# Kernel tuning notes

Hardware: AMD Instinct MI355X
Metric: run time of the kernel (lower is better)

Reference implementation:

```python
import jax, jax.numpy as jnp
import numpy as np
import math

B, N, D, H = 4, 2048, 1024, 16
HD = D // H  # head dim = 64


def setup_inputs() -> dict:
    key = jax.random.key(0)
    ks = jax.random.split(key, 5)
    x = jax.random.normal(ks[0], (B, N, D), dtype=jnp.float32)
    # per-head kqv Linear: weight (3*HD, D), bias (3*HD), stacked over heads
    Wkqv = jax.random.normal(ks[1], (H, 3 * HD, D), dtype=jnp.float32) / math.sqrt(D)
    bkqv = jax.random.normal(ks[2], (H, 3 * HD), dtype=jnp.float32) * 0.02
    # output projection Linear(D, D)
    Wproj = jax.random.normal(ks[3], (D, D), dtype=jnp.float32) / math.sqrt(D)
    bproj = jax.random.normal(ks[4], (D,), dtype=jnp.float32) * 0.02
    return {"x": x, "Wkqv": Wkqv, "bkqv": bkqv, "Wproj": Wproj, "bproj": bproj}


def reference(x, Wkqv, bkqv, Wproj, bproj):
    # per-head linear: y = x @ W.T + b  -> [B, H, N, 3*HD]
    kqv = jnp.einsum('bnd,hed->bhne', x, Wkqv) + bkqv[None, :, None, :]
    k, q, v = jnp.split(kqv, 3, axis=-1)  # each [B, H, N, HD]
    # scores = q @ k^T / sqrt(HD)   (attention_scores(k, q) -> q @ k.T)
    scores = jnp.einsum('bhqd,bhkd->bhqk', q, k) / math.sqrt(HD)
    causal = jnp.tril(jnp.ones((N, N), dtype=bool))
    scores = jnp.where(causal[None, None], scores, -jnp.inf)
    att = jax.nn.softmax(scores, axis=-1)
    out = jnp.einsum('bhqk,bhkd->bhqd', att, v)  # [B, H, N, HD]
    # concat heads: [B, N, H*HD]
    sa = out.transpose(0, 2, 1, 3).reshape(B, N, D)
    # dropout is identity in eval mode; final projection
    return sa @ Wproj.T + bproj
```

## Files before the change

kernel.cpp:

```cpp
#include <hip/hip_runtime.h>
#include <hip/hip_bf16.h>


#define NSEQ 2048
#define NHEAD 16
#define DMODEL 1024
#define SCALE2 0.18033688011112042f

typedef __attribute__((ext_vector_type(8))) short v8s;
typedef __attribute__((ext_vector_type(4))) float v4f;

__device__ __forceinline__ float bf2f(unsigned short u) {
    union { unsigned int i; float f; } v;
    v.i = ((unsigned int)u) << 16;
    return v.f;
}
__device__ __forceinline__ unsigned short f2bf(float f) {
    unsigned int x = __float_as_uint(f);
    return (unsigned short)((x + 0x7fffu + ((x >> 16) & 1u)) >> 16);
}
__device__ __forceinline__ unsigned short f2bf_rh(float f) {
    return (unsigned short)((__float_as_uint(f) + 0x8000u) >> 16);
}
__device__ __forceinline__ float fast_exp2(float x) {
#if __has_builtin(__builtin_amdgcn_exp2f)
    return __builtin_amdgcn_exp2f(x);
#else
    return __expf(x * 0.69314718056f);
#endif
}
__device__ __forceinline__ void gld_lds16(const unsigned short* g, unsigned short* l) {
    __builtin_amdgcn_global_load_lds(
        (const __attribute__((address_space(1))) void*)g,
        (__attribute__((address_space(3))) void*)l, 16, 0, 0);
}

__global__ __launch_bounds__(256) void cvt_bf16(
    const float* __restrict__ x, const float* __restrict__ wk, const float* __restrict__ wp,
    unsigned short* __restrict__ xb, unsigned short* __restrict__ wkb,
    unsigned short* __restrict__ wpb)
{
    const int i = blockIdx.x * 256 + threadIdx.x;
    const float* s; unsigned short* d; int o;
    if (i < 2097152)      { s = x;  d = xb;  o = i; }
    else if (i < 2883584) {
        s = wk; d = wkb;
        const int oi  = i - 2097152;
        const int row = oi >> 8, cq = oi & 255;
        const int h   = row / 192;
        const int rem = row - h * 192;
        const int cls = rem >> 6, e = rem & 63;
        float4 f = ((const float4*)s)[oi];
        ushort4 u;
        u.x = f2bf(f.x); u.y = f2bf(f.y); u.z = f2bf(f.z); u.w = f2bf(f.w);
        ((ushort4*)d)[(((cls << 10) + (h << 6) + e) << 8) + cq] = u;
        return;
    }
    else                  { s = wp; d = wpb; o = i - 2883584; }
    float4 f = ((const float4*)s)[o];
    ushort4 u;
    u.x = f2bf(f.x); u.y = f2bf(f.y); u.z = f2bf(f.z); u.w = f2bf(f.w);
    ((ushort4*)d)[o] = u;
}

template <int EPI>
__global__ __launch_bounds__(512, 2) void gemm_lds(
    const unsigned short* __restrict__ A, const unsigned short* __restrict__ B,
    const float* __restrict__ bias,
    float* __restrict__ Cf,
    unsigned short* __restrict__ Kb, unsigned short* __restrict__ Qb,
    unsigned short* __restrict__ VTb,
    int M, int Nc, int K)
{
    __shared__ __align__(16) unsigned short Al[4][8192];
    __shared__ __align__(16) unsigned short Bl[4][8192];

    const int t = threadIdx.x, wave = t >> 6, lane = t & 63;
    const int wm = wave >> 2, wn = wave & 3;

    const int lin = blockIdx.y * gridDim.x + blockIdx.x;
    const int xcd = lin & 7, pos = lin >> 3;
    const int by  = (xcd << 2) + (pos & 3);
    const int bx  = pos >> 2;
    const int m0 = by * 256, n0 = bx * 256;
    const int quad = lane >> 4, c = lane & 15;

    const int g0 = wave * 2, g1 = wave * 2 + 1;
    const int r15 = lane & 15, kg = (lane >> 4) & 3;
    const unsigned short* sA0 = A + (size_t)(m0 + g0 * 16 + r15) * K + kg * 8;
    const unsigned short* sA1 = A + (size_t)(m0 + g1 * 16 + r15) * K + kg * 8;
    const unsigned short* sB0 = B + (size_t)(n0 + g0 * 16 + r15) * K + kg * 8;
    const unsigned short* sB1 = B + (size_t)(n0 + g1 * 16 + r15) * K + kg * 8;

    v4f acc[8][4];
#pragma unroll
    for (int i = 0; i < 8; ++i)
#pragma unroll
        for (int j = 0; j < 4; ++j) acc[i][j] = (v4f){0.f, 0.f, 0.f, 0.f};

    const int fbase = (quad * 16 + c) * 8;
    const int nt = K >> 5;

    auto stageA = [&](int sl, int tt) {
        const int o = tt << 5;
        unsigned short* la = &Al[sl][0];
        gld_lds16(sA0 + o, la + g0 * 512);
        gld_lds16(sA1 + o, la + g1 * 512);
    };
    auto stageB = [&](int sl, int tt) {
        const int o = tt << 5;
        unsigned short* lb = &Bl[sl][0];
        gld_lds16(sB0 + o, lb + g0 * 512);
        gld_lds16(sB1 + o, lb + g1 * 512);
    };

    stageA(0, 0); stageB(0, 0);
    stageA(1, 1); stageB(1, 1);
    stageA(2, 2); stageB(2, 2);
    asm volatile("s_waitcnt vmcnt(8)" ::: "memory");
    __builtin_amdgcn_s_barrier();

    for (int tt = 0; tt < nt; ++tt) {
        const int sl  = tt & 3;
        const int sl3 = (tt + 3) & 3;
        const bool pf = (tt + 3 < nt);

        v8s bfr[4], af[4];
#pragma unroll
        for (int ns = 0; ns < 4; ++ns)
            bfr[ns] = *(const v8s*)&Bl[sl][(wn * 4 + ns) * 512 + fbase];
#pragma unroll
        for (int ms = 0; ms < 4; ++ms)
            af[ms] = *(const v8s*)&Al[sl][(wm * 8 + ms) * 512 + fbase];
        if (pf) stageA(sl3, tt + 3);
        __builtin_amdgcn_s_barrier();
        asm volatile("s_waitcnt lgkmcnt(0)" ::: "memory");
        __builtin_amdgcn_s_setprio(1);
#pragma unroll
        for (int ms = 0; ms < 4; ++ms)
#pragma unroll
            for (int ns = 0; ns < 4; ++ns)
                acc[ms][ns] = __builtin_amdgcn_mfma_f32_16x16x32_bf16(
                    af[ms], bfr[ns], acc[ms][ns], 0, 0, 0);
        __builtin_amdgcn_s_setprio(0);
        __builtin_amdgcn_s_barrier();

        v8s af2[4];
#pragma unroll
        for (int ms = 0; ms < 4; ++ms)
            af2[ms] = *(const v8s*)&Al[sl][(wm * 8 + 4 + ms) * 512 + fbase];
        if (pf) stageB(sl3, tt + 3);
        __builtin_amdgcn_s_barrier();
        asm volatile("s_waitcnt lgkmcnt(0)" ::: "memory");
        __builtin_amdgcn_s_setprio(1);
#pragma unroll
        for (int ms = 0; ms < 4; ++ms)
#pragma unroll
            for (int ns = 0; ns < 4; ++ns)
                acc[4 + ms][ns] = __builtin_amdgcn_mfma_f32_16x16x32_bf16(
                    af2[ms], bfr[ns], acc[4 + ms][ns], 0, 0, 0);
        __builtin_amdgcn_s_setprio(0);
        if (pf)                   { asm volatile("s_waitcnt vmcnt(8)" ::: "memory"); }
        else if (tt + 2 < nt)     { asm volatile("s_waitcnt vmcnt(4)" ::: "memory"); }
        else                      { asm volatile("s_waitcnt vmcnt(0)" ::: "memory"); }
        __builtin_amdgcn_s_barrier();
    }

#pragma unroll
    for (int ms = 0; ms < 8; ++ms) {
        const int row0 = m0 + wm * 128 + ms * 16 + quad * 4;
#pragma unroll
        for (int ns = 0; ns < 4; ++ns) {
            const int colbase = n0 + wn * 64 + ns * 16;
            float bn, scl = 1.f;
            if (EPI == 2) {
                bn = bias[colbase + c];
            } else {
                const int cls = colbase >> 10;
                const int wi  = colbase & 1023;
                const int h   = wi >> 6, e0 = wi & 63;
                bn = bias[h * 192 + cls * 64 + e0 + c];
                if (cls == 1) scl = SCALE2;
            }
            float v0 = (acc[ms][ns][0] + bn) * scl;
            float v1 = (acc[ms][ns][1] + bn) * scl;
            float v2 = (acc[ms][ns][2] + bn) * scl;
            float v3 = (acc[ms][ns][3] + bn) * scl;
            if (EPI == 2) {
                float* pc = Cf + (size_t)row0 * Nc + colbase + c;
                pc[0] = v0; pc[(size_t)Nc] = v1;
                pc[(size_t)2 * Nc] = v2; pc[(size_t)3 * Nc] = v3;
            } else {
                const int cls = colbase >> 10;
                const int wi  = colbase & 1023;
                const int h   = wi >> 6, e = (wi & 63) + c;
                const int bb  = row0 >> 11, tok0 = row0 & 2047;
                const int bhh = bb * 16 + h;
                if (cls == 2) {
                    ushort4 pk;
                    pk.x = f2bf(v0); pk.y = f2bf(v1); pk.z = f2bf(v2); pk.w = f2bf(v3);
                    *(ushort4*)(VTb + ((size_t)bhh * 64 + e) * 2048 + tok0) = pk;
                } else {
                    unsigned short* dst = (cls == 0) ? Kb : Qb;
                    const size_t base = ((size_t)bhh * 2048 + tok0) * 64 + e;
                    dst[base]       = f2bf(v0);
                    dst[base + 64]  = f2bf(v1);
                    dst[base + 128] = f2bf(v2);
                    dst[base + 192] = f2bf(v3);
                }
            }
        }
    }
}

template <bool A_BF16, int EPI>
__global__ __launch_bounds__(256) void gemm_mfma(
    const void* __restrict__ Av, const float* __restrict__ B,
    const float* __restrict__ bias,
    float* __restrict__ Cf,
    unsigned short* __restrict__ Kb, unsigned short* __restrict__ Qb,
    unsigned short* __restrict__ VTb,
    int M, int Nc, int K)
{
    __shared__ __align__(16) unsigned short Al[512 * 8];
    __shared__ __align__(16) unsigned short Bl[512 * 8];

    const int t = threadIdx.x;
    const int wave = t >> 6, lane = t & 63;
    const int wm = wave >> 1, wn = wave & 1;
    const int m0 = blockIdx.y * 128, n0 = blockIdx.x * 128;
    const int quad = lane >> 4, c = lane & 15;

    const int srow = t >> 1, skh = t & 1;
    const int sslot = (srow >> 4) * 64 + (skh * 2) * 16 + (srow & 15);

    v4f acc[4][4];
#pragma unroll
    for (int i = 0; i < 4; ++i)
#pragma unroll
        for (int j = 0; j < 4; ++j) acc[i][j] = (v4f){0.f, 0.f, 0.f, 0.f};

    const unsigned short* pa_u = (const unsigned short*)Av + (size_t)(m0 + srow) * K + skh * 16;
    const float*          pa_f = (const float*)Av          + (size_t)(m0 + srow) * K + skh * 16;
    const float*          pb   = B                          + (size_t)(n0 + srow) * K + skh * 16;

    const int fbase = (quad * 16 + c) * 8;

    for (int k0 = 0; k0 < K; k0 += 32) {
        unsigned short a16[16], b16[16];
        if (A_BF16) {
            uint4 r0 = *(const uint4*)(pa_u + k0);
            uint4 r1 = *(const uint4*)(pa_u + k0 + 8);
            *(uint4*)&a16[0] = r0; *(uint4*)&a16[8] = r1;
        } else {
            float4 f0 = *(const float4*)(pa_f + k0);
            float4 f1 = *(const float4*)(pa_f + k0 + 4);
            float4 f2 = *(const float4*)(pa_f + k0 + 8);
            float4 f3 = *(const float4*)(pa_f + k0 + 12);
            a16[0] = f2bf_rh(f0.x); a16[1] = f2bf_rh(f0.y); a16[2] = f2bf_rh(f0.z); a16[3] = f2bf_rh(f0.w);
            a16[4] = f2bf_rh(f1.x); a16[5] = f2bf_rh(f1.y); a16[6] = f2bf_rh(f1.z); a16[7] = f2bf_rh(f1.w);
            a16[8] = f2bf_rh(f2.x); a16[9] = f2bf_rh(f2.y); a16[10] = f2bf_rh(f2.z); a16[11] = f2bf_rh(f2.w);
            a16[12] = f2bf_rh(f3.x); a16[13] = f2bf_rh(f3.y); a16[14] = f2bf_rh(f3.z); a16[15] = f2bf_rh(f3.w);
        }
        {
            float4 g0 = *(const float4*)(pb + k0);
            float4 g1 = *(const float4*)(pb + k0 + 4);
            float4 g2 = *(const float4*)(pb + k0 + 8);
            float4 g3 = *(const float4*)(pb + k0 + 12);
            b16[0] = f2bf_rh(g0.x); b16[1] = f2bf_rh(g0.y); b16[2] = f2bf_rh(g0.z); b16[3] = f2bf_rh(g0.w);
            b16[4] = f2bf_rh(g1.x); b16[5] = f2bf_rh(g1.y); b16[6] = f2bf_rh(g1.z); b16[7] = f2bf_rh(g1.w);
            b16[8] = f2bf_rh(g2.x); b16[9] = f2bf_rh(g2.y); b16[10] = f2bf_rh(g2.z); b16[11] = f2bf_rh(g2.w);
            b16[12] = f2bf_rh(g3.x); b16[13] = f2bf_rh(g3.y); b16[14] = f2bf_rh(g3.z); b16[15] = f2bf_rh(g3.w);
        }
        __syncthreads();
        *(uint4*)&Al[sslot * 8]        = *(uint4*)&a16[0];
        *(uint4*)&Al[(sslot + 16) * 8] = *(uint4*)&a16[8];
        *(uint4*)&Bl[sslot * 8]        = *(uint4*)&b16[0];
        *(uint4*)&Bl[(sslot + 16) * 8] = *(uint4*)&b16[8];
        __syncthreads();

        v8s af[4], bf[4];
#pragma unroll
        for (int ms = 0; ms < 4; ++ms)
            af[ms] = *(const v8s*)&Al[(wm * 4 + ms) * 512 + fbase];
#pragma unroll
        for (int ns = 0; ns < 4; ++ns)
            bf[ns] = *(const v8s*)&Bl[(wn * 4 + ns) * 512 + fbase];
#pragma unroll
        for (int ms = 0; ms < 4; ++ms)
#pragma unroll
            for (int ns = 0; ns < 4; ++ns)
                acc[ms][ns] = __builtin_amdgcn_mfma_f32_16x16x32_bf16(
                    af[ms], bf[ns], acc[ms][ns], 0, 0, 0);
    }

#pragma unroll
    for (int ms = 0; ms < 4; ++ms) {
        const int row0 = m0 + wm * 64 + ms * 16 + quad * 4;
#pragma unroll
        for (int ns = 0; ns < 4; ++ns) {
            const int colbase = n0 + wn * 64 + ns * 16;
            float bn = (EPI == 2) ? bias[colbase + c] : bias[colbase + c];
            float v0 = acc[ms][ns][0] + bn;
            float v1 = acc[ms][ns][1] + bn;
            float v2 = acc[ms][ns][2] + bn;
            float v3 = acc[ms][ns][3] + bn;
            if (EPI == 2) {
                float* pc = Cf + (size_t)row0 * Nc + colbase + c;
                pc[0] = v0; pc[(size_t)Nc] = v1;
                pc[(size_t)2 * Nc] = v2; pc[(size_t)3 * Nc] = v3;
            } else {
                const int hh = colbase / 192;
                const int eb = colbase - hh * 192;
                const int bb = row0 >> 11, tok0 = row0 & 2047;
                const int bhh = bb * 16 + hh;
                if (eb >= 128) {
                    ushort4 pk;
                    pk.x = f2bf(v0); pk.y = f2bf(v1); pk.z = f2bf(v2); pk.w = f2bf(v3);
                    *(ushort4*)(VTb + ((size_t)bhh * 64 + (eb - 128) + c) * 2048 + tok0) = pk;
                } else {
                    const bool isq = (eb >= 64);
                    const float s = isq ? SCALE2 : 1.f;
                    unsigned short* dst = isq ? Qb : Kb;
                    const int e = (isq ? eb - 64 : eb) + c;
                    const size_t base = ((size_t)bhh * 2048 + tok0) * 64 + e;
                    dst[base]       = f2bf(v0 * s);
                    dst[base + 64]  = f2bf(v1 * s);
                    dst[base + 128] = f2bf(v2 * s);
                    dst[base + 192] = f2bf(v3 * s);
                }
            }
        }
    }
}

#define ATTS 72

__global__ __launch_bounds__(256, 2) void attn_mfma(
    const unsigned short* __restrict__ Kbuf,
    const unsigned short* __restrict__ Qbuf,
    const unsigned short* __restrict__ VT,
    unsigned short* __restrict__ sa)
{
    __shared__ __align__(16) unsigned short Ps[4][2][64 * ATTS];

    const int t = threadIdx.x, w = t >> 6, lane = t & 63;
    const int quad = lane >> 4, c = lane & 15;
    const int bh = blockIdx.x & 63, bq = blockIdx.x >> 6;
    const int b = bh >> 4, hh = bh & 15;
    const int qt = (w == 0) ? bq : (w == 1) ? (15 - bq) : (w == 2) ? (16 + bq) : (31 - bq);
    const int qw = qt * 64;
    const size_t gbase = (size_t)bh * (2048 * 64);

    const int rs  = c & 3;
    const int rc0 = (quad ^ rs) * 8, rc1 = 32 + rc0;
    unsigned short* PsW0 = &Ps[w][0][0];
    unsigned short* PsW1 = &Ps[w][1][0];

    v8s qf[4][2];
#pragma unroll
    for (int qs = 0; qs < 4; ++qs) {
        const unsigned short* qp = Qbuf + gbase + (size_t)(qw + qs * 16 + c) * 64 + quad * 8;
        qf[qs][0] = *(const v8s*)qp;
        qf[qs][1] = *(const v8s*)(qp + 32);
    }
    v4f oacc[4][4], lacc[4];
#pragma unroll
    for (int qs = 0; qs < 4; ++qs) {
        lacc[qs] = (v4f){0.f, 0.f, 0.f, 0.f};
#pragma unroll
        for (int dn = 0; dn < 4; ++dn) oacc[qs][dn] = (v4f){0.f, 0.f, 0.f, 0.f};
    }
    const short oneb = (short)0x3F80;
    const v8s ones = {oneb, oneb, oneb, oneb, oneb, oneb, oneb, oneb};

    const int nkt = qt + 1;
    for (int kt = 0; kt < nkt; ++kt) {
        const int kbase = kt * 64;
        const bool diag = (kt == nkt - 1);
        unsigned short* PsW = (kt & 1) ? PsW1 : PsW0;

        v8s vf[4][2];
#pragma unroll
        for (int dn = 0; dn < 4; ++dn) {
            const unsigned short* vp =
                VT + gbase + (size_t)(dn * 16 + c) * 2048 + kbase + quad * 8;
            vf[dn][0] = *(const v8s*)vp;
            vf[dn][1] = *(const v8s*)(vp + 32);
        }

#pragma unroll
        for (int kn = 0; kn < 4; ++kn) {
            const unsigned short* kp =
                Kbuf + gbase + (size_t)(kbase + kn * 16 + c) * 64 + quad * 8;
            v8s kf0 = *(const v8s*)kp;
            v8s kf1 = *(const v8s*)(kp + 32);
#pragma unroll
            for (int qs = 0; qs < 4; ++qs) {
                v4f s = (v4f){0.f, 0.f, 0.f, 0.f};
                s = __builtin_amdgcn_mfma_f32_16x16x32_bf16(qf[qs][0], kf0, s, 0, 0, 0);
                s = __builtin_amdgcn_mfma_f32_16x16x32_bf16(qf[qs][1], kf1, s, 0, 0, 0);
                if (diag) {
#pragma unroll
                    for (int r = 0; r < 4; ++r)
                        if (kn * 16 + c > qs * 16 + quad * 4 + r) s[r] = -1e30f;
                }
#pragma unroll
                for (int r = 0; r < 4; ++r) {
                    const float p = fast_exp2(s[r]);
                    PsW[(qs * 16 + quad * 4 + r) * ATTS +
                        (((2 * kn + (c >> 3)) ^ r) * 8) + (c & 7)] = f2bf_rh(p);
                }
            }
        }
        v8s pa[4][2];
#pragma unroll
        for (int qs = 0; qs < 4; ++qs) {
            pa[qs][0] = *(const v8s*)&PsW[(qs * 16 + c) * ATTS + rc0];
            pa[qs][1] = *(const v8s*)&PsW[(qs * 16 + c) * ATTS + rc1];
        }
#pragma unroll
        for (int dn = 0; dn < 4; ++dn) {
#pragma unroll
            for (int qs = 0; qs < 4; ++qs) {
                oacc[qs][dn] = __builtin_amdgcn_mfma_f32_16x16x32_bf16(pa[qs][0], vf[dn][0], oacc[qs][dn], 0, 0, 0);
                oacc[qs][dn] = __builtin_amdgcn_mfma_f32_16x16x32_bf16(pa[qs][1], vf[dn][1], oacc[qs][dn], 0, 0, 0);
            }
        }
#pragma unroll
        for (int qs = 0; qs < 4; ++qs) {
            lacc[qs] = __builtin_amdgcn_mfma_f32_16x16x32_bf16(pa[qs][0], ones, lacc[qs], 0, 0, 0);
            lacc[qs] = __builtin_amdgcn_mfma_f32_16x16x32_bf16(pa[qs][1], ones, lacc[qs], 0, 0, 0);
        }
    }

#pragma unroll
    for (int qs = 0; qs < 4; ++qs) {
        float inv[4];
#pragma unroll
        for (int r = 0; r < 4; ++r) inv[r] = 1.f / lacc[qs][r];
        const size_t obase =
            ((size_t)(b * 2048 + qw + qs * 16 + quad * 4)) * DMODEL + hh * 64;
#pragma unroll
        for (int dn = 0; dn < 4; ++dn)
#pragma unroll
            for (int r = 0; r < 4; ++r)
                sa[obase + (size_t)r * DMODEL + dn * 16 + c] = f2bf(oacc[qs][dn][r] * inv[r]);
    }
}

extern "C" void kernel_launch(void* const* d_in, const int* in_sizes, int n_in,
                              void* d_out, int out_size, void* d_ws, size_t ws_size,
                              hipStream_t stream) {
    const float* x     = (const float*)d_in[0];
    const float* Wkqv  = (const float*)d_in[1];
    const float* bkqv  = (const float*)d_in[2];
    const float* Wproj = (const float*)d_in[3];
    const float* bproj = (const float*)d_in[4];
    float* out = (float*)d_out;

    unsigned short* Kb = (unsigned short*)d_ws;
    unsigned short* Qb = Kb + (size_t)8388608;
    unsigned short* VT = Qb + (size_t)8388608;
    unsigned short* sa = VT + (size_t)8388608;

    const bool fast = ws_size >= 75497472ull;
    if (fast) {
        unsigned short* xb  = sa;
        unsigned short* wkb = (unsigned short*)d_ws + (size_t)33554432;
        unsigned short* wpb = wkb + (size_t)3145728;
        cvt_bf16<<<12288, 256, 0, stream>>>(x, Wkqv, Wproj, xb, wkb, wpb);
        gemm_lds<1><<<dim3(12, 32), 512, 0, stream>>>(
            xb, wkb, bkqv, nullptr, Kb, Qb, VT, 8192, 3072, 1024);
        attn_mfma<<<512, 256, 0, stream>>>(Kb, Qb, VT, sa);
        gemm_lds<2><<<dim3(4, 32), 512, 0, stream>>>(
            sa, wpb, bproj, out, nullptr, nullptr, nullptr, 8192, 1024, 1024);
    } else {
        gemm_mfma<false, 1><<<dim3(24, 64), 256, 0, stream>>>(
            x, Wkqv, bkqv, nullptr, Kb, Qb, VT, 8192, 3072, 1024);
        attn_mfma<<<512, 256, 0, stream>>>(Kb, Qb, VT, sa);
        gemm_mfma<true, 2><<<dim3(8, 64), 256, 0, stream>>>(
            sa, Wproj, bproj, out, nullptr, nullptr, nullptr, 8192, 1024, 1024);
    }
}
```

Before: 305.5 us.

## Split long causal query tiles across waves to balance per-wave attention work

In the attention kernel, waves 2 and 3 now only process key tiles 0–16 for their long query tiles. Waves 0 and 1, after finishing their own short tiles, compute the remaining key tiles for those long query tiles. Partial unnormalized outputs and row sums are merged through shared memory with one block barrier, so per-wave work is roughly equal instead of being set by the longest causal row. This costs extra LDS for the merge buffer and a __syncthreads. To offset the added LDS, the P staging buffer drops from double to single buffering.

```diff
diff --git a/kernel.cpp b/kernel.cpp
--- a/kernel.cpp
+++ b/kernel.cpp
@@ -342,110 +342,148 @@
     const unsigned short* __restrict__ VT,
     unsigned short* __restrict__ sa)
 {
-    __shared__ __align__(16) unsigned short Ps[4][2][64 * ATTS];
+    __shared__ __align__(16) unsigned short Ps[4][64 * ATTS];
+    __shared__ __align__(16) float Mrg[2][64][81];
 
     const int t = threadIdx.x, w = t >> 6, lane = t & 63;
     const int quad = lane >> 4, c = lane & 15;
     const int bh = blockIdx.x & 63, bq = blockIdx.x >> 6;
     const int b = bh >> 4, hh = bh & 15;
-    const int qt = (w == 0) ? bq : (w == 1) ? (15 - bq) : (w == 2) ? (16 + bq) : (31 - bq);
-    const int qw = qt * 64;
     const size_t gbase = (size_t)bh * (2048 * 64);
 
     const int rs  = c & 3;
     const int rc0 = (quad ^ rs) * 8, rc1 = 32 + rc0;
-    unsigned short* PsW0 = &Ps[w][0][0];
-    unsigned short* PsW1 = &Ps[w][1][0];
-
-    v8s qf[4][2];
-#pragma unroll
-    for (int qs = 0; qs < 4; ++qs) {
-        const unsigned short* qp = Qbuf + gbase + (size_t)(qw + qs * 16 + c) * 64 + quad * 8;
-        qf[qs][0] = *(const v8s*)qp;
-        qf[qs][1] = *(const v8s*)(qp + 32);
-    }
+    unsigned short* PsW = &Ps[w][0];
+
+    const int qtA = (w == 0) ? bq : (w == 1) ? (15 - bq) : (w == 2) ? (16 + bq) : (31 - bq);
+    const int kA1 = (w == 0) ? (bq + 1) : (w == 1) ? (16 - bq) : 17;
+    const int qtB = (w == 0) ? (31 - bq) : (16 + bq);
+    const int kB1 = (w == 0) ? (32 - bq) : (17 + bq);
+
     v4f oacc[4][4], lacc[4];
-#pragma unroll
-    for (int qs = 0; qs < 4; ++qs) {
-        lacc[qs] = (v4f){0.f, 0.f, 0.f, 0.f};
-#pragma unroll
-        for (int dn = 0; dn < 4; ++dn) oacc[qs][dn] = (v4f){0.f, 0.f, 0.f, 0.f};
-    }
     const short oneb = (short)0x3F80;
     const v8s ones = {oneb, oneb, oneb, oneb, oneb, oneb, oneb, oneb};
 
-    const int nkt = qt + 1;
-    for (int kt = 0; kt < nkt; ++kt) {
-        const int kbase = kt * 64;
-        const bool diag = (kt == nkt - 1);
-        unsigned short* PsW = (kt & 1) ? PsW1 : PsW0;
-
-        v8s vf[4][2];
-#pragma unroll
-        for (int dn = 0; dn < 4; ++dn) {
-            const unsigned short* vp =
-                VT + gbase + (size_t)(dn * 16 + c) * 2048 + kbase + quad * 8;
-            vf[dn][0] = *(const v8s*)vp;
-            vf[dn][1] = *(const v8s*)(vp + 32);
-        }
-
-#pragma unroll
-        for (int kn = 0; kn < 4; ++kn) {
-            const unsigned short* kp =
-                Kbuf + gbase + (size_t)(kbase + kn * 16 + c) * 64 + quad * 8;
-            v8s kf0 = *(const v8s*)kp;
-            v8s kf1 = *(const v8s*)(kp + 32);
+    auto run_seg = [&](int qt, int k0, int k1) {
+        const int qw = qt * 64;
+        v8s qf[4][2];
+#pragma unroll
+        for (int qs = 0; qs < 4; ++qs) {
+            const unsigned short* qp =
+                Qbuf + gbase + (size_t)(qw + qs * 16 + c) * 64 + quad * 8;
+            qf[qs][0] = *(const v8s*)qp;
+            qf[qs][1] = *(const v8s*)(qp + 32);
+        }
+#pragma unroll
+        for (int qs = 0; qs < 4; ++qs) {
+            lacc[qs] = (v4f){0.f, 0.f, 0.f, 0.f};
+#pragma unroll
+            for (int dn = 0; dn < 4; ++dn) oacc[qs][dn] = (v4f){0.f, 0.f, 0.f, 0.f};
+        }
+        for (int kt = k0; kt < k1; ++kt) {
+            const int kbase = kt * 64;
+            const bool diag = (kt == qt);
+
+            v8s vf[4][2];
+#pragma unroll
+            for (int dn = 0; dn < 4; ++dn) {
+                const unsigned short* vp =
+                    VT + gbase + (size_t)(dn * 16 + c) * 2048 + kbase + quad * 8;
+                vf[dn][0] = *(const v8s*)vp;
+                vf[dn][1] = *(const v8s*)(vp + 32);
+            }
+
+#pragma unroll
+            for (int kn = 0; kn < 4; ++kn) {
+                const unsigned short* kp =
+                    Kbuf + gbase + (size_t)(kbase + kn * 16 + c) * 64 + quad * 8;
+                v8s kf0 = *(const v8s*)kp;
+                v8s kf1 = *(const v8s*)(kp + 32);
+#pragma unroll
+                for (int qs = 0; qs < 4; ++qs) {
+                    v4f s = (v4f){0.f, 0.f, 0.f, 0.f};
+                    s = __builtin_amdgcn_mfma_f32_16x16x32_bf16(qf[qs][0], kf0, s, 0, 0, 0);
+                    s = __builtin_amdgcn_mfma_f32_16x16x32_bf16(qf[qs][1], kf1, s, 0, 0, 0);
+                    if (diag) {
+#pragma unroll
+                        for (int r = 0; r < 4; ++r)
+                            if (kn * 16 + c > qs * 16 + quad * 4 + r) s[r] = -1e30f;
+                    }
+#pragma unroll
+                    for (int r = 0; r < 4; ++r) {
+                        const float p = fast_exp2(s[r]);
+                        PsW[(qs * 16 + quad * 4 + r) * ATTS +
+                            (((2 * kn + (c >> 3)) ^ r) * 8) + (c & 7)] = f2bf_rh(p);
+                    }
+                }
+            }
+            v8s pa[4][2];
 #pragma unroll
             for (int qs = 0; qs < 4; ++qs) {
-                v4f s = (v4f){0.f, 0.f, 0.f, 0.f};
-                s = __builtin_amdgcn_mfma_f32_16x16x32_bf16(qf[qs][0], kf0, s, 0, 0, 0);
-                s = __builtin_amdgcn_mfma_f32_16x16x32_bf16(qf[qs][1], kf1, s, 0, 0, 0);
-                if (diag) {
-#pragma unroll
-                    for (int r = 0; r < 4; ++r)
-                        if (kn * 16 + c > qs * 16 + quad * 4 + r) s[r] = -1e30f;
+                pa[qs][0] = *(const v8s*)&PsW[(qs * 16 + c) * ATTS + rc0];
+                pa[qs][1] = *(const v8s*)&PsW[(qs * 16 + c) * ATTS + rc1];
+            }
+#pragma unroll
+            for (int dn = 0; dn < 4; ++dn) {
+#pragma unroll
+                for (int qs = 0; qs < 4; ++qs) {
+                    oacc[qs][dn] = __builtin_amdgcn_mfma_f32_16x16x32_bf16(pa[qs][0], vf[dn][0], oacc[qs][dn], 0, 0, 0);
+                    oacc[qs][dn] = __builtin_amdgcn_mfma_f32_16x16x32_bf16(pa[qs][1], vf[dn][1], oacc[qs][dn], 0, 0, 0);
                 }
-#pragma unroll
-                for (int r = 0; r < 4; ++r) {
-                    const float p = fast_exp2(s[r]);
-                    PsW[(qs * 16 + quad * 4 + r) * ATTS +
-                        (((2 * kn + (c >> 3)) ^ r) * 8) + (c & 7)] = f2bf_rh(p);
-                }
-            }
-        }
-        v8s pa[4][2];
+            }
+#pragma unroll
+            for (int qs = 0; qs < 4; ++qs) {
+                lacc[qs] = __builtin_amdgcn_mfma_f32_16x16x32_bf16(pa[qs][0], ones, lacc[qs], 0, 0, 0);
+                lacc[qs] = __builtin_amdgcn_mfma_f32_16x16x32_bf16(pa[qs][1], ones, lacc[qs], 0, 0, 0);
+            }
+        }
+    };
+
+    auto store_final = [&](int qt) {
+        const int qw = qt * 64;
 #pragma unroll
         for (int qs = 0; qs < 4; ++qs) {
-            pa[qs][0] = *(const v8s*)&PsW[(qs * 16 + c) * ATTS + rc0];
-            pa[qs][1] = *(const v8s*)&PsW[(qs * 16 + c) * ATTS + rc1];
-        }
-#pragma unroll
-        for (int dn = 0; dn < 4; ++dn) {
-#pragma unroll
-            for (int qs = 0; qs < 4; ++qs) {
-                oacc[qs][dn] = __builtin_amdgcn_mfma_f32_16x16x32_bf16(pa[qs][0], vf[dn][0], oacc[qs][dn], 0, 0, 0);
-                oacc[qs][dn] = __builtin_amdgcn_mfma_f32_16x16x32_bf16(pa[qs][1], vf[dn][1], oacc[qs][dn], 0, 0, 0);
-            }
-        }
+            float inv[4];
+#pragma unroll
+            for (int r = 0; r < 4; ++r) inv[r] = 1.f / lacc[qs][r];
+            const size_t obase =
+                ((size_t)(b * 2048 + qw + qs * 16 + quad * 4)) * DMODEL + hh * 64;
+#pragma unroll
+            for (int dn = 0; dn < 4; ++dn)
+#pragma unroll
+                for (int r = 0; r < 4; ++r)
+                    sa[obase + (size_t)r * DMODEL + dn * 16 + c] = f2bf(oacc[qs][dn][r] * inv[r]);
+        }
+    };
+
+    run_seg(qtA, 0, kA1);
+    if (w < 2) {
+        store_final(qtA);
+        run_seg(qtB, 17, kB1);
+        float* mg = &Mrg[w][lane][0];
 #pragma unroll
         for (int qs = 0; qs < 4; ++qs) {
-            lacc[qs] = __builtin_amdgcn_mfma_f32_16x16x32_bf16(pa[qs][0], ones, lacc[qs], 0, 0, 0);
-            lacc[qs] = __builtin_amdgcn_mfma_f32_16x16x32_bf16(pa[qs][1], ones, lacc[qs], 0, 0, 0);
-        }
-    }
-
-#pragma unroll
-    for (int qs = 0; qs < 4; ++qs) {
-        float inv[4];
-#pragma unroll
-        for (int r = 0; r < 4; ++r) inv[r] = 1.f / lacc[qs][r];
-        const size_t obase =
-            ((size_t)(b * 2048 + qw + qs * 16 + quad * 4)) * DMODEL + hh * 64;
-#pragma unroll
-        for (int dn = 0; dn < 4; ++dn)
-#pragma unroll
-            for (int r = 0; r < 4; ++r)
-                sa[obase + (size_t)r * DMODEL + dn * 16 + c] = f2bf(oacc[qs][dn][r] * inv[r]);
+#pragma unroll
+            for (int dn = 0; dn < 4; ++dn)
+#pragma unroll
+                for (int r = 0; r < 4; ++r) mg[qs * 16 + dn * 4 + r] = oacc[qs][dn][r];
+#pragma unroll
+            for (int r = 0; r < 4; ++r) mg[64 + qs * 4 + r] = lacc[qs][r];
+        }
+    }
+    __syncthreads();
+    if (w >= 2) {
+        const float* mg = &Mrg[3 - w][lane][0];
+#pragma unroll
+        for (int qs = 0; qs < 4; ++qs) {
+#pragma unroll
+            for (int dn = 0; dn < 4; ++dn)
+#pragma unroll
+                for (int r = 0; r < 4; ++r) oacc[qs][dn][r] += mg[qs * 16 + dn * 4 + r];
+#pragma unroll
+            for (int r = 0; r < 4; ++r) lacc[qs][r] += mg[64 + qs * 4 + r];
+        }
+        store_final(qtA);
     }
 }
 
```

Result: faster. 291.6 us (-4.6%).
